# Optimization experiments

Hardware: AMD Instinct MI355X
Metric: run time of the kernel (lower is better)

Reference implementation:

```python
import jax, jax.numpy as jnp
import numpy as np

MARGIN = 1.0
EPS = 1e-6  # torch F.pairwise_distance default eps, added elementwise to (x - y)
NEG_INF = -1e30
POS_INF = 1e30


def _pairwise_dist_matrix(e):
    # D[i,j] = || e_i - e_j + EPS ||_2, expanded so we never materialize [B,B,D]:
    # ||d + eps||^2 = ||d||^2 + 2*eps*sum(d) + Dfeat*eps^2,  d = e_i - e_j
    sq = jnp.sum(e * e, axis=1)          # [B]
    s = jnp.sum(e, axis=1)               # [B]
    d2 = (sq[:, None] + sq[None, :] - 2.0 * (e @ e.T)
          + 2.0 * EPS * (s[:, None] - s[None, :])
          + e.shape[1] * (EPS * EPS))
    return jnp.sqrt(jnp.maximum(d2, 0.0))  # [B,B]


def _pdist(x, y):
    # F.pairwise_distance(p=2): ||x - y + eps||
    return jnp.sqrt(jnp.sum(jnp.square(x - y + EPS), axis=-1))


def setup_inputs() -> dict:
    B, D = 4096, 128
    key = jax.random.key(0)
    k1, k2, k3, k4 = jax.random.split(key, 4)
    embedding = jax.random.normal(k1, (B, D), dtype=jnp.float32)
    # label space == batch, each label appears exactly once in the batch
    target_idx = jax.random.permutation(k2, B).astype(jnp.int32)
    positive_idxs = jax.random.bernoulli(k3, 0.02, (B, B))  # [B, L] label-space mask
    negative_idxs = jax.random.bernoulli(k4, 0.5, (B, B))
    return {"embedding": embedding, "target_idx": target_idx,
            "positive_idxs": positive_idxs, "negative_idxs": negative_idxs}


def reference(embedding, target_idx, positive_idxs, negative_idxs):
    # Mining happens under no_grad in the original module.
    dm = jax.lax.stop_gradient(_pairwise_dist_matrix(embedding))  # [B,B]
    # batch j is a positive/negative candidate for anchor i iff its label is flagged
    pos_mask = positive_idxs[:, target_idx]  # [B,B] bool
    neg_mask = negative_idxs[:, target_idx]
    pos_idx = jnp.argmax(jnp.where(pos_mask, dm, NEG_INF), axis=1)  # hardest positive
    neg_idx = jnp.argmin(jnp.where(neg_mask, dm, POS_INF), axis=1)  # hardest negative
    valid = jnp.any(pos_mask, axis=1) & jnp.any(neg_mask, axis=1)
    a = embedding
    p = embedding[pos_idx]
    n = embedding[neg_idx]
    ap = _pdist(a, p)
    an = _pdist(a, n)
    pn = _pdist(p, n)
    loss = jax.nn.relu(ap - jnp.minimum(an, pn) + MARGIN)
    w = valid.astype(loss.dtype)
    return jnp.sum(loss * w) / jnp.maximum(jnp.sum(w), 1.0)
```

## Files before the change

kernel.cpp:

```cpp
#include <hip/hip_runtime.h>
#include <stdint.h>

#define BN 4096
#define DD 128
#define EPSF 1e-6f
#define MARGINF 1.0f
#define TM 128
#define TN 128
#define KC 64
#define CHUNK 256

typedef unsigned long long ull;

__device__ __forceinline__ unsigned int ord_f32(float f) {
    unsigned int u = __float_as_uint(f);
    return (u & 0x80000000u) ? ~u : (u | 0x80000000u);
}

__global__ void k_prep(const float* __restrict__ e, const int* __restrict__ tidx,
                       float* __restrict__ sq, float* __restrict__ s,
                       int* __restrict__ inv,
                       ull* __restrict__ pk, ull* __restrict__ nk) {
    int wid = threadIdx.x >> 6;
    int lane = threadIdx.x & 63;
    int row = blockIdx.x * 4 + wid;
    float2 v = ((const float2*)(e + (size_t)row * DD))[lane];
    float ss = v.x + v.y;
    float qq = v.x * v.x + v.y * v.y;
    #pragma unroll
    for (int off = 32; off > 0; off >>= 1) {
        ss += __shfl_down(ss, off);
        qq += __shfl_down(qq, off);
    }
    if (lane == 0) {
        sq[row] = qq; s[row] = ss;
        inv[tidx[row]] = row;
        pk[row] = 0ULL; nk[row] = ~0ULL;
    }
}

__global__ __launch_bounds__(256, 2)
void k_select(const float* __restrict__ e,
              const int* __restrict__ pos, const int* __restrict__ neg,
              const float* __restrict__ sq, const float* __restrict__ s,
              const int* __restrict__ inv,
              ull* __restrict__ pkey, ull* __restrict__ nkey) {
    __shared__ float Al[KC][TM];
    __shared__ float Bl[KC][TN];
    __shared__ float ri[TM];
    __shared__ float rj[CHUNK];
    __shared__ int   jvs[CHUNK];

    const int tid = threadIdx.x;
    const int tx = tid & 15, ty = tid >> 4;
    const int i0 = blockIdx.x * TM;
    const int c0 = blockIdx.y * CHUNK;

    for (int t = tid; t < CHUNK; t += 256) {
        int j = inv[c0 + t];
        jvs[t] = j;
        rj[t] = sq[j] - 2.0f * EPSF * s[j];
    }
    if (tid < TM) ri[tid] = sq[i0 + tid] + 2.0f * EPSF * s[i0 + tid];

    float bpv[8], bnv[8]; int bpi[8], bni[8];
    #pragma unroll
    for (int r = 0; r < 8; r++) {
        bpv[r] = -3.4e38f; bnv[r] = 3.4e38f;
        bpi[r] = 0x7FFFFFFF; bni[r] = 0x7FFFFFFF;
    }

    for (int jt = 0; jt < CHUNK / TN; jt++) {
        float acc[8][8];
        #pragma unroll
        for (int r = 0; r < 8; r++)
            #pragma unroll
            for (int c = 0; c < 8; c++) acc[r][c] = 0.0f;

        for (int kc = 0; kc < DD / KC; kc++) {
            __syncthreads();
            for (int it = 0; it < 8; ++it) {
                int id = it * 256 + tid;
                int grp = id >> 2, kk = id & 3;
                int row = grp & (TM - 1);
                int kq = ((grp >> 7) << 2) + kk;
                float4 v = ((const float4*)(e + (size_t)(i0 + row) * DD + kc * KC))[kq];
                int k = kq * 4;
                Al[k + 0][row] = v.x; Al[k + 1][row] = v.y;
                Al[k + 2][row] = v.z; Al[k + 3][row] = v.w;
            }
            for (int it = 0; it < 8; ++it) {
                int id = it * 256 + tid;
                int grp = id >> 2, kk = id & 3;
                int rr = grp & (TN - 1);
                int kq = ((grp >> 7) << 2) + kk;
                int jrow = jvs[jt * TN + rr];
                float4 v = ((const float4*)(e + (size_t)jrow * DD + kc * KC))[kq];
                int k = kq * 4;
                Bl[k + 0][rr] = v.x; Bl[k + 1][rr] = v.y;
                Bl[k + 2][rr] = v.z; Bl[k + 3][rr] = v.w;
            }
            __syncthreads();

            #pragma unroll 2
            for (int k = 0; k < KC; k++) {
                float4 a0 = *(const float4*)&Al[k][ty * 8];
                float4 a1 = *(const float4*)&Al[k][ty * 8 + 4];
                float4 b0 = *(const float4*)&Bl[k][tx * 8];
                float4 b1 = *(const float4*)&Bl[k][tx * 8 + 4];
                float av[8] = {a0.x, a0.y, a0.z, a0.w, a1.x, a1.y, a1.z, a1.w};
                float bv[8] = {b0.x, b0.y, b0.z, b0.w, b1.x, b1.y, b1.z, b1.w};
                #pragma unroll
                for (int r = 0; r < 8; r++)
                    #pragma unroll
                    for (int c = 0; c < 8; c++)
                        acc[r][c] = fmaf(av[r], bv[c], acc[r][c]);
            }
        }

        const int cbase = c0 + jt * TN;
        float rjv[8]; int jjv[8];
        #pragma unroll
        for (int c = 0; c < 8; c++) {
            int jl = jt * TN + tx * 8 + c;
            rjv[c] = rj[jl];
            jjv[c] = jvs[jl];
        }
        #pragma unroll
        for (int r = 0; r < 8; r++) {
            int irow = ty * 8 + r;
            const int* pr = pos + (size_t)(i0 + irow) * BN + cbase + tx * 8;
            const int* nr = neg + (size_t)(i0 + irow) * BN + cbase + tx * 8;
            int4 pm0 = ((const int4*)pr)[0], pm1 = ((const int4*)pr)[1];
            int4 nm0 = ((const int4*)nr)[0], nm1 = ((const int4*)nr)[1];
            int pmv[8] = {pm0.x, pm0.y, pm0.z, pm0.w, pm1.x, pm1.y, pm1.z, pm1.w};
            int nmv[8] = {nm0.x, nm0.y, nm0.z, nm0.w, nm1.x, nm1.y, nm1.z, nm1.w};
            float riv = ri[irow];
            #pragma unroll
            for (int c = 0; c < 8; c++) {
                float d2 = riv + rjv[c] - 2.0f * acc[r][c] + (float)DD * EPSF * EPSF;
                int j = jjv[c];
                if (pmv[c] != 0) {
                    if (d2 > bpv[r] || (d2 == bpv[r] && j < bpi[r])) { bpv[r] = d2; bpi[r] = j; }
                }
                if (nmv[c] != 0) {
                    if (d2 < bnv[r] || (d2 == bnv[r] && j < bni[r])) { bnv[r] = d2; bni[r] = j; }
                }
            }
        }
    }

    __syncthreads();
    float* spv = &Bl[0][0];
    int*   spi = (int*)(spv + 2048);
    float* snv = (float*)(spi + 2048);
    int*   sni = (int*)(snv + 2048);
    #pragma unroll
    for (int r = 0; r < 8; r++) {
        int row = ty * 8 + r;
        spv[row * 16 + tx] = bpv[r]; spi[row * 16 + tx] = bpi[r];
        snv[row * 16 + tx] = bnv[r]; sni[row * 16 + tx] = bni[r];
    }
    __syncthreads();
    if (tid < TM) {
        float bv = -3.4e38f, nv = 3.4e38f;
        int bi = 0x7FFFFFFF, ni = 0x7FFFFFFF;
        for (int t = 0; t < 16; t++) {
            float v = spv[tid * 16 + t]; int ix = spi[tid * 16 + t];
            if (ix != 0x7FFFFFFF && (v > bv || (v == bv && ix < bi))) { bv = v; bi = ix; }
            v = snv[tid * 16 + t]; ix = sni[tid * 16 + t];
            if (ix != 0x7FFFFFFF && (v < nv || (v == nv && ix < ni))) { nv = v; ni = ix; }
        }
        if (bi != 0x7FFFFFFF) {
            ull key = ((ull)ord_f32(bv) << 32) | (ull)(0xFFFFFFFFu - (unsigned)bi);
            atomicMax(&pkey[i0 + tid], key);
        }
        if (ni != 0x7FFFFFFF) {
            ull key = ((ull)ord_f32(nv) << 32) | (ull)(unsigned)ni;
            atomicMin(&nkey[i0 + tid], key);
        }
    }
}

__global__ void k_loss(const float* __restrict__ e,
                       const ull* __restrict__ pkey, const ull* __restrict__ nkey,
                       float* __restrict__ partials) {
    int tid = threadIdx.x;
    int row = blockIdx.x * 256 + tid;
    ull pk = pkey[row], nk = nkey[row];
    float loss = 0.0f, w = 0.0f;
    if (pk != 0ULL && nk != ~0ULL) {
        int pi = (int)(0xFFFFFFFFu - (unsigned)(pk & 0xFFFFFFFFu));
        int ni = (int)(unsigned)(nk & 0xFFFFFFFFu);
        const float4* a4 = (const float4*)(e + (size_t)row * DD);
        const float4* p4 = (const float4*)(e + (size_t)pi * DD);
        const float4* n4 = (const float4*)(e + (size_t)ni * DD);
        float ap2 = 0.0f, an2 = 0.0f, pn2 = 0.0f;
        #pragma unroll 8
        for (int k = 0; k < DD / 4; k++) {
            float4 a = a4[k], p = p4[k], n = n4[k];
            float d;
            d = a.x - p.x + EPSF; ap2 = fmaf(d, d, ap2);
            d = a.y - p.y + EPSF; ap2 = fmaf(d, d, ap2);
            d = a.z - p.z + EPSF; ap2 = fmaf(d, d, ap2);
            d = a.w - p.w + EPSF; ap2 = fmaf(d, d, ap2);
            d = a.x - n.x + EPSF; an2 = fmaf(d, d, an2);
            d = a.y - n.y + EPSF; an2 = fmaf(d, d, an2);
            d = a.z - n.z + EPSF; an2 = fmaf(d, d, an2);
            d = a.w - n.w + EPSF; an2 = fmaf(d, d, an2);
            d = p.x - n.x + EPSF; pn2 = fmaf(d, d, pn2);
            d = p.y - n.y + EPSF; pn2 = fmaf(d, d, pn2);
            d = p.z - n.z + EPSF; pn2 = fmaf(d, d, pn2);
            d = p.w - n.w + EPSF; pn2 = fmaf(d, d, pn2);
        }
        float ap = sqrtf(ap2), an = sqrtf(an2), pn = sqrtf(pn2);
        loss = fmaxf(ap - fminf(an, pn) + MARGINF, 0.0f);
        w = 1.0f;
    }
    __shared__ float sl[4], sw[4];
    int wid = tid >> 6, lane = tid & 63;
    #pragma unroll
    for (int off = 32; off > 0; off >>= 1) {
        loss += __shfl_down(loss, off);
        w    += __shfl_down(w, off);
    }
    if (lane == 0) { sl[wid] = loss; sw[wid] = w; }
    __syncthreads();
    if (tid == 0) {
        float L = sl[0] + sl[1] + sl[2] + sl[3];
        float W = sw[0] + sw[1] + sw[2] + sw[3];
        partials[blockIdx.x * 2 + 0] = L;
        partials[blockIdx.x * 2 + 1] = W;
    }
}

__global__ void k_final(const float* __restrict__ partials, float* __restrict__ out) {
    float L = 0.0f, W = 0.0f;
    for (int b = 0; b < BN / 256; b++) { L += partials[2 * b]; W += partials[2 * b + 1]; }
    out[0] = L / fmaxf(W, 1.0f);
}

extern "C" void kernel_launch(void* const* d_in, const int* in_sizes, int n_in,
                              void* d_out, int out_size, void* d_ws, size_t ws_size,
                              hipStream_t stream) {
    const float* e    = (const float*)d_in[0];
    const int*   tidx = (const int*)d_in[1];
    const int*   pos  = (const int*)d_in[2];
    const int*   neg  = (const int*)d_in[3];
    float* out = (float*)d_out;

    ull*   pkey = (ull*)d_ws;
    ull*   nkey = pkey + BN;
    float* sq   = (float*)(nkey + BN);
    float* s    = sq + BN;
    int*   inv  = (int*)(s + BN);
    float* partials = (float*)(inv + BN);

    k_prep<<<BN / 4, 256, 0, stream>>>(e, tidx, sq, s, inv, pkey, nkey);
    dim3 grid(BN / TM, BN / CHUNK);
    k_select<<<grid, 256, 0, stream>>>(e, pos, neg, sq, s, inv, pkey, nkey);
    k_loss<<<BN / 256, 256, 0, stream>>>(e, pkey, nkey, partials);
    k_final<<<1, 1, 0, stream>>>(partials, out);
}
```

Baseline: 224.3 us.

## Use split-bf16 MFMA for distance GEMM, bit-pack masks, warp-parallel loss

Replaces the scalar fp32 FMA Gram-matrix computation with MFMA bf16 instructions, using a three-term hi/lo split to approximate fp32 accuracy. A separate pass packs the int32 pos/neg masks into 64-bit ballot bitmasks, so the selection kernel reads bits instead of full ints. The loss kernel now uses one wavefront per row, and the final reduction becomes parallel. The split-bf16 product may differ slightly from fp32 and can flip argmax/argmin ties. The mask packing still reads the full masks once, but in a separate pass.

```diff
diff --git a/kernel.cpp b/kernel.cpp
--- a/kernel.cpp
+++ b/kernel.cpp
@@ -8,23 +8,33 @@
 #define TM 128
 #define TN 128
 #define KC 64
-#define CHUNK 256
 
 typedef unsigned long long ull;
+typedef short short8 __attribute__((ext_vector_type(8)));
+typedef float f32x4 __attribute__((ext_vector_type(4)));
 
 __device__ __forceinline__ unsigned int ord_f32(float f) {
     unsigned int u = __float_as_uint(f);
     return (u & 0x80000000u) ? ~u : (u | 0x80000000u);
 }
+__device__ __forceinline__ unsigned short bf16_rne(float x) {
+    unsigned int u = __float_as_uint(x);
+    return (unsigned short)((u + 0x7FFFu + ((u >> 16) & 1u)) >> 16);
+}
 
 __global__ void k_prep(const float* __restrict__ e, const int* __restrict__ tidx,
                        float* __restrict__ sq, float* __restrict__ s,
-                       int* __restrict__ inv,
-                       ull* __restrict__ pk, ull* __restrict__ nk) {
-    int wid = threadIdx.x >> 6;
-    int lane = threadIdx.x & 63;
-    int row = blockIdx.x * 4 + wid;
+                       int* __restrict__ inv, ull* __restrict__ pk, ull* __restrict__ nk,
+                       unsigned int* __restrict__ ehi, unsigned int* __restrict__ elo) {
+    int w = threadIdx.x >> 6, lane = threadIdx.x & 63;
+    int row = blockIdx.x * 4 + w;
     float2 v = ((const float2*)(e + (size_t)row * DD))[lane];
+    unsigned short hx = bf16_rne(v.x), hy = bf16_rne(v.y);
+    float rx = v.x - __uint_as_float((unsigned int)hx << 16);
+    float ry = v.y - __uint_as_float((unsigned int)hy << 16);
+    unsigned short lx = bf16_rne(rx), ly = bf16_rne(ry);
+    ehi[row * 64 + lane] = (unsigned int)hx | ((unsigned int)hy << 16);
+    elo[row * 64 + lane] = (unsigned int)lx | ((unsigned int)ly << 16);
     float ss = v.x + v.y;
     float qq = v.x * v.x + v.y * v.y;
     #pragma unroll
@@ -39,119 +49,160 @@
     }
 }
 
+__global__ void k_bits(const int* __restrict__ pos, const int* __restrict__ neg,
+                       ull* __restrict__ pb, ull* __restrict__ nb) {
+    int row = blockIdx.x;
+    int w = threadIdx.x >> 6, lane = threadIdx.x & 63;
+    const int* pr = pos + (size_t)row * BN;
+    const int* nr = neg + (size_t)row * BN;
+    #pragma unroll 4
+    for (int g = 0; g < 16; g++) {
+        int col = g * 256 + w * 64 + lane;
+        ull b = __ballot(pr[col] != 0);
+        if (lane == 0) pb[row * 64 + g * 4 + w] = b;
+        b = __ballot(nr[col] != 0);
+        if (lane == 0) nb[row * 64 + g * 4 + w] = b;
+    }
+}
+
 __global__ __launch_bounds__(256, 2)
-void k_select(const float* __restrict__ e,
-              const int* __restrict__ pos, const int* __restrict__ neg,
+void k_select(const unsigned short* __restrict__ ehi, const unsigned short* __restrict__ elo,
               const float* __restrict__ sq, const float* __restrict__ s,
               const int* __restrict__ inv,
+              const ull* __restrict__ pbits, const ull* __restrict__ nbits,
               ull* __restrict__ pkey, ull* __restrict__ nkey) {
-    __shared__ float Al[KC][TM];
-    __shared__ float Bl[KC][TN];
-    __shared__ float ri[TM];
-    __shared__ float rj[CHUNK];
-    __shared__ int   jvs[CHUNK];
+    __shared__ __align__(16) char smem[73728];
+    __shared__ int   jvs[TN];
+    __shared__ float ri[TM], rj[TN];
+    __shared__ ull   pbl[256], nbl[256];
+
+    unsigned short* Ah = (unsigned short*)smem;
+    unsigned short* Alo = Ah + 9216;
+    unsigned short* Bh = Ah + 18432;
+    unsigned short* Blo = Ah + 27648;
+    float* Dl = (float*)smem;
 
     const int tid = threadIdx.x;
+    const int i0 = blockIdx.x * TM;
+    const int c0 = blockIdx.y * TN;
+
+    if (tid < TN) {
+        int j = inv[c0 + tid];
+        jvs[tid] = j;
+        rj[tid] = sq[j] - 2.0f * EPSF * s[j];
+        ri[tid] = sq[i0 + tid] + 2.0f * EPSF * s[i0 + tid];
+    }
+    {
+        int irow = tid >> 1, half = tid & 1;
+        size_t bidx = (size_t)(i0 + irow) * 64 + (c0 >> 6) + half;
+        pbl[tid] = pbits[bidx];
+        nbl[tid] = nbits[bidx];
+    }
+
+    const int lane = tid & 63, w = tid >> 6;
+    const int lrow = lane & 15, quad = lane >> 4;
+
+    f32x4 acc[2][8];
+    #pragma unroll
+    for (int rt = 0; rt < 2; rt++)
+        #pragma unroll
+        for (int ct = 0; ct < 8; ct++)
+            acc[rt][ct] = (f32x4){0.f, 0.f, 0.f, 0.f};
+
+    for (int kc = 0; kc < DD / KC; kc++) {
+        __syncthreads();
+        {
+            int rr0 = tid >> 3, seg = tid & 7;
+            #pragma unroll
+            for (int p = 0; p < 4; p++) {
+                int rr = p * 32 + rr0;
+                int ar = i0 + rr;
+                int jr = jvs[rr];
+                int4 va = ((const int4*)(ehi + (size_t)ar * DD))[kc * 8 + seg];
+                int4 vb = ((const int4*)(elo + (size_t)ar * DD))[kc * 8 + seg];
+                *(int4*)(Ah + rr * 72 + seg * 8) = va;
+                *(int4*)(Alo + rr * 72 + seg * 8) = vb;
+                va = ((const int4*)(ehi + (size_t)jr * DD))[kc * 8 + seg];
+                vb = ((const int4*)(elo + (size_t)jr * DD))[kc * 8 + seg];
+                *(int4*)(Bh + rr * 72 + seg * 8) = va;
+                *(int4*)(Blo + rr * 72 + seg * 8) = vb;
+            }
+        }
+        __syncthreads();
+
+        #pragma unroll
+        for (int ks = 0; ks < 2; ks++) {
+            const int kof = ks * 32 + quad * 8;
+            short8 ahi[2], alo2[2];
+            #pragma unroll
+            for (int rt = 0; rt < 2; rt++) {
+                const unsigned short* ap = Ah + (w * 32 + rt * 16 + lrow) * 72 + kof;
+                const unsigned short* lp = Alo + (w * 32 + rt * 16 + lrow) * 72 + kof;
+                ahi[rt] = *(const short8*)ap;
+                alo2[rt] = *(const short8*)lp;
+            }
+            #pragma unroll
+            for (int ct = 0; ct < 8; ct++) {
+                const unsigned short* bp = Bh + (ct * 16 + lrow) * 72 + kof;
+                const unsigned short* blp = Blo + (ct * 16 + lrow) * 72 + kof;
+                short8 bhi = *(const short8*)bp;
+                short8 blo = *(const short8*)blp;
+                #pragma unroll
+                for (int rt = 0; rt < 2; rt++) {
+                    acc[rt][ct] = __builtin_amdgcn_mfma_f32_16x16x32_bf16(ahi[rt], bhi, acc[rt][ct], 0, 0, 0);
+                    acc[rt][ct] = __builtin_amdgcn_mfma_f32_16x16x32_bf16(ahi[rt], blo, acc[rt][ct], 0, 0, 0);
+                    acc[rt][ct] = __builtin_amdgcn_mfma_f32_16x16x32_bf16(alo2[rt], bhi, acc[rt][ct], 0, 0, 0);
+                }
+            }
+        }
+    }
+
+    __syncthreads();
+    #pragma unroll
+    for (int rt = 0; rt < 2; rt++)
+        #pragma unroll
+        for (int ct = 0; ct < 8; ct++) {
+            int rbase = w * 32 + rt * 16 + quad * 4;
+            int col = ct * 16 + lrow;
+            #pragma unroll
+            for (int t = 0; t < 4; t++)
+                Dl[(rbase + t) * 132 + col] = acc[rt][ct][t];
+        }
+    __syncthreads();
+
     const int tx = tid & 15, ty = tid >> 4;
-    const int i0 = blockIdx.x * TM;
-    const int c0 = blockIdx.y * CHUNK;
-
-    for (int t = tid; t < CHUNK; t += 256) {
-        int j = inv[c0 + t];
-        jvs[t] = j;
-        rj[t] = sq[j] - 2.0f * EPSF * s[j];
-    }
-    if (tid < TM) ri[tid] = sq[i0 + tid] + 2.0f * EPSF * s[i0 + tid];
-
     float bpv[8], bnv[8]; int bpi[8], bni[8];
     #pragma unroll
     for (int r = 0; r < 8; r++) {
         bpv[r] = -3.4e38f; bnv[r] = 3.4e38f;
         bpi[r] = 0x7FFFFFFF; bni[r] = 0x7FFFFFFF;
     }
-
-    for (int jt = 0; jt < CHUNK / TN; jt++) {
-        float acc[8][8];
-        #pragma unroll
-        for (int r = 0; r < 8; r++)
-            #pragma unroll
-            for (int c = 0; c < 8; c++) acc[r][c] = 0.0f;
-
-        for (int kc = 0; kc < DD / KC; kc++) {
-            __syncthreads();
-            for (int it = 0; it < 8; ++it) {
-                int id = it * 256 + tid;
-                int grp = id >> 2, kk = id & 3;
-                int row = grp & (TM - 1);
-                int kq = ((grp >> 7) << 2) + kk;
-                float4 v = ((const float4*)(e + (size_t)(i0 + row) * DD + kc * KC))[kq];
-                int k = kq * 4;
-                Al[k + 0][row] = v.x; Al[k + 1][row] = v.y;
-                Al[k + 2][row] = v.z; Al[k + 3][row] = v.w;
-            }
-            for (int it = 0; it < 8; ++it) {
-                int id = it * 256 + tid;
-                int grp = id >> 2, kk = id & 3;
-                int rr = grp & (TN - 1);
-                int kq = ((grp >> 7) << 2) + kk;
-                int jrow = jvs[jt * TN + rr];
-                float4 v = ((const float4*)(e + (size_t)jrow * DD + kc * KC))[kq];
-                int k = kq * 4;
-                Bl[k + 0][rr] = v.x; Bl[k + 1][rr] = v.y;
-                Bl[k + 2][rr] = v.z; Bl[k + 3][rr] = v.w;
-            }
-            __syncthreads();
-
-            #pragma unroll 2
-            for (int k = 0; k < KC; k++) {
-                float4 a0 = *(const float4*)&Al[k][ty * 8];
-                float4 a1 = *(const float4*)&Al[k][ty * 8 + 4];
-                float4 b0 = *(const float4*)&Bl[k][tx * 8];
-                float4 b1 = *(const float4*)&Bl[k][tx * 8 + 4];
-                float av[8] = {a0.x, a0.y, a0.z, a0.w, a1.x, a1.y, a1.z, a1.w};
-                float bv[8] = {b0.x, b0.y, b0.z, b0.w, b1.x, b1.y, b1.z, b1.w};
-                #pragma unroll
-                for (int r = 0; r < 8; r++)
-                    #pragma unroll
-                    for (int c = 0; c < 8; c++)
-                        acc[r][c] = fmaf(av[r], bv[c], acc[r][c]);
-            }
-        }
-
-        const int cbase = c0 + jt * TN;
-        float rjv[8]; int jjv[8];
+    const int shift = (tx & 7) * 8;
+    #pragma unroll
+    for (int r = 0; r < 8; r++) {
+        int irow = ty * 8 + r;
+        float4 d0 = *(const float4*)&Dl[irow * 132 + tx * 8];
+        float4 d1 = *(const float4*)&Dl[irow * 132 + tx * 8 + 4];
+        float dot[8] = {d0.x, d0.y, d0.z, d0.w, d1.x, d1.y, d1.z, d1.w};
+        unsigned int pb = (unsigned int)((pbl[irow * 2 + (tx >> 3)] >> shift) & 0xFFu);
+        unsigned int nb = (unsigned int)((nbl[irow * 2 + (tx >> 3)] >> shift) & 0xFFu);
+        float riv = ri[irow];
         #pragma unroll
         for (int c = 0; c < 8; c++) {
-            int jl = jt * TN + tx * 8 + c;
-            rjv[c] = rj[jl];
-            jjv[c] = jvs[jl];
-        }
-        #pragma unroll
-        for (int r = 0; r < 8; r++) {
-            int irow = ty * 8 + r;
-            const int* pr = pos + (size_t)(i0 + irow) * BN + cbase + tx * 8;
-            const int* nr = neg + (size_t)(i0 + irow) * BN + cbase + tx * 8;
-            int4 pm0 = ((const int4*)pr)[0], pm1 = ((const int4*)pr)[1];
-            int4 nm0 = ((const int4*)nr)[0], nm1 = ((const int4*)nr)[1];
-            int pmv[8] = {pm0.x, pm0.y, pm0.z, pm0.w, pm1.x, pm1.y, pm1.z, pm1.w};
-            int nmv[8] = {nm0.x, nm0.y, nm0.z, nm0.w, nm1.x, nm1.y, nm1.z, nm1.w};
-            float riv = ri[irow];
-            #pragma unroll
-            for (int c = 0; c < 8; c++) {
-                float d2 = riv + rjv[c] - 2.0f * acc[r][c] + (float)DD * EPSF * EPSF;
-                int j = jjv[c];
-                if (pmv[c] != 0) {
-                    if (d2 > bpv[r] || (d2 == bpv[r] && j < bpi[r])) { bpv[r] = d2; bpi[r] = j; }
-                }
-                if (nmv[c] != 0) {
-                    if (d2 < bnv[r] || (d2 == bnv[r] && j < bni[r])) { bnv[r] = d2; bni[r] = j; }
-                }
-            }
-        }
-    }
-
-    __syncthreads();
-    float* spv = &Bl[0][0];
+            int jl = tx * 8 + c;
+            float d2 = riv + rj[jl] - 2.0f * dot[c] + (float)DD * EPSF * EPSF;
+            int j = jvs[jl];
+            if ((pb >> c) & 1u) {
+                if (d2 > bpv[r] || (d2 == bpv[r] && j < bpi[r])) { bpv[r] = d2; bpi[r] = j; }
+            }
+            if ((nb >> c) & 1u) {
+                if (d2 < bnv[r] || (d2 == bnv[r] && j < bni[r])) { bnv[r] = d2; bni[r] = j; }
+            }
+        }
+    }
+
+    __syncthreads();
+    float* spv = (float*)smem;
     int*   spi = (int*)(spv + 2048);
     float* snv = (float*)(spi + 2048);
     int*   sni = (int*)(snv + 2048);
@@ -185,59 +236,66 @@
 __global__ void k_loss(const float* __restrict__ e,
                        const ull* __restrict__ pkey, const ull* __restrict__ nkey,
                        float* __restrict__ partials) {
-    int tid = threadIdx.x;
-    int row = blockIdx.x * 256 + tid;
+    int w = threadIdx.x >> 6, lane = threadIdx.x & 63;
+    int row = blockIdx.x * 4 + w;
     ull pk = pkey[row], nk = nkey[row];
-    float loss = 0.0f, w = 0.0f;
+    float loss = 0.0f, wt = 0.0f;
     if (pk != 0ULL && nk != ~0ULL) {
         int pi = (int)(0xFFFFFFFFu - (unsigned)(pk & 0xFFFFFFFFu));
         int ni = (int)(unsigned)(nk & 0xFFFFFFFFu);
-        const float4* a4 = (const float4*)(e + (size_t)row * DD);
-        const float4* p4 = (const float4*)(e + (size_t)pi * DD);
-        const float4* n4 = (const float4*)(e + (size_t)ni * DD);
-        float ap2 = 0.0f, an2 = 0.0f, pn2 = 0.0f;
-        #pragma unroll 8
-        for (int k = 0; k < DD / 4; k++) {
-            float4 a = a4[k], p = p4[k], n = n4[k];
-            float d;
-            d = a.x - p.x + EPSF; ap2 = fmaf(d, d, ap2);
-            d = a.y - p.y + EPSF; ap2 = fmaf(d, d, ap2);
-            d = a.z - p.z + EPSF; ap2 = fmaf(d, d, ap2);
-            d = a.w - p.w + EPSF; ap2 = fmaf(d, d, ap2);
-            d = a.x - n.x + EPSF; an2 = fmaf(d, d, an2);
-            d = a.y - n.y + EPSF; an2 = fmaf(d, d, an2);
-            d = a.z - n.z + EPSF; an2 = fmaf(d, d, an2);
-            d = a.w - n.w + EPSF; an2 = fmaf(d, d, an2);
-            d = p.x - n.x + EPSF; pn2 = fmaf(d, d, pn2);
-            d = p.y - n.y + EPSF; pn2 = fmaf(d, d, pn2);
-            d = p.z - n.z + EPSF; pn2 = fmaf(d, d, pn2);
-            d = p.w - n.w + EPSF; pn2 = fmaf(d, d, pn2);
-        }
-        float ap = sqrtf(ap2), an = sqrtf(an2), pn = sqrtf(pn2);
-        loss = fmaxf(ap - fminf(an, pn) + MARGINF, 0.0f);
-        w = 1.0f;
+        float2 av = ((const float2*)(e + (size_t)row * DD))[lane];
+        float2 pv = ((const float2*)(e + (size_t)pi * DD))[lane];
+        float2 nv = ((const float2*)(e + (size_t)ni * DD))[lane];
+        float dx, dy;
+        dx = av.x - pv.x + EPSF; dy = av.y - pv.y + EPSF;
+        float ap2 = dx * dx + dy * dy;
+        dx = av.x - nv.x + EPSF; dy = av.y - nv.y + EPSF;
+        float an2 = dx * dx + dy * dy;
+        dx = pv.x - nv.x + EPSF; dy = pv.y - nv.y + EPSF;
+        float pn2 = dx * dx + dy * dy;
+        #pragma unroll
+        for (int off = 32; off > 0; off >>= 1) {
+            ap2 += __shfl_down(ap2, off);
+            an2 += __shfl_down(an2, off);
+            pn2 += __shfl_down(pn2, off);
+        }
+        if (lane == 0) {
+            float ap = sqrtf(ap2), an = sqrtf(an2), pn = sqrtf(pn2);
+            loss = fmaxf(ap - fminf(an, pn) + MARGINF, 0.0f);
+            wt = 1.0f;
+        }
     }
     __shared__ float sl[4], sw[4];
-    int wid = tid >> 6, lane = tid & 63;
+    if (lane == 0) { sl[w] = loss; sw[w] = wt; }
+    __syncthreads();
+    if (threadIdx.x == 0) {
+        partials[blockIdx.x * 2 + 0] = sl[0] + sl[1] + sl[2] + sl[3];
+        partials[blockIdx.x * 2 + 1] = sw[0] + sw[1] + sw[2] + sw[3];
+    }
+}
+
+__global__ void k_final(const float* __restrict__ partials, float* __restrict__ out) {
+    int tid = threadIdx.x;
+    float L = 0.0f, W = 0.0f;
+    for (int i = 0; i < 4; i++) {
+        int idx = tid + i * 256;
+        L += partials[idx * 2];
+        W += partials[idx * 2 + 1];
+    }
     #pragma unroll
     for (int off = 32; off > 0; off >>= 1) {
-        loss += __shfl_down(loss, off);
-        w    += __shfl_down(w, off);
-    }
-    if (lane == 0) { sl[wid] = loss; sw[wid] = w; }
+        L += __shfl_down(L, off);
+        W += __shfl_down(W, off);
+    }
+    __shared__ float sl[4], sw[4];
+    int w = tid >> 6, lane = tid & 63;
+    if (lane == 0) { sl[w] = L; sw[w] = W; }
     __syncthreads();
     if (tid == 0) {
-        float L = sl[0] + sl[1] + sl[2] + sl[3];
-        float W = sw[0] + sw[1] + sw[2] + sw[3];
-        partials[blockIdx.x * 2 + 0] = L;
-        partials[blockIdx.x * 2 + 1] = W;
-    }
-}
-
-__global__ void k_final(const float* __restrict__ partials, float* __restrict__ out) {
-    float L = 0.0f, W = 0.0f;
-    for (int b = 0; b < BN / 256; b++) { L += partials[2 * b]; W += partials[2 * b + 1]; }
-    out[0] = L / fmaxf(W, 1.0f);
+        float Lt = sl[0] + sl[1] + sl[2] + sl[3];
+        float Wt = sw[0] + sw[1] + sw[2] + sw[3];
+        out[0] = Lt / fmaxf(Wt, 1.0f);
+    }
 }
 
 extern "C" void kernel_launch(void* const* d_in, const int* in_sizes, int n_in,
@@ -249,16 +307,22 @@
     const int*   neg  = (const int*)d_in[3];
     float* out = (float*)d_out;
 
-    ull*   pkey = (ull*)d_ws;
-    ull*   nkey = pkey + BN;
-    float* sq   = (float*)(nkey + BN);
-    float* s    = sq + BN;
-    int*   inv  = (int*)(s + BN);
+    ull* pkey  = (ull*)d_ws;
+    ull* nkey  = pkey + BN;
+    ull* pbits = nkey + BN;
+    ull* nbits = pbits + BN * 64;
+    float* sq  = (float*)(nbits + BN * 64);
+    float* s   = sq + BN;
+    int* inv   = (int*)(s + BN);
     float* partials = (float*)(inv + BN);
-
-    k_prep<<<BN / 4, 256, 0, stream>>>(e, tidx, sq, s, inv, pkey, nkey);
-    dim3 grid(BN / TM, BN / CHUNK);
-    k_select<<<grid, 256, 0, stream>>>(e, pos, neg, sq, s, inv, pkey, nkey);
-    k_loss<<<BN / 256, 256, 0, stream>>>(e, pkey, nkey, partials);
-    k_final<<<1, 1, 0, stream>>>(partials, out);
-}
+    unsigned int* ehi = (unsigned int*)(partials + 2048);
+    unsigned int* elo = ehi + BN * 64;
+
+    k_prep<<<BN / 4, 256, 0, stream>>>(e, tidx, sq, s, inv, pkey, nkey, ehi, elo);
+    k_bits<<<BN, 256, 0, stream>>>(pos, neg, pbits, nbits);
+    dim3 grid(BN / TM, BN / TN);
+    k_select<<<grid, 256, 0, stream>>>((const unsigned short*)ehi, (const unsigned short*)elo,
+                                       sq, s, inv, pbits, nbits, pkey, nkey);
+    k_loss<<<BN / 4, 256, 0, stream>>>(e, pkey, nkey, partials);
+    k_final<<<1, 256, 0, stream>>>(partials, out);
+}
```

After: 209.2 us. 1.07x faster.
